# Optimization experiments

Measured on AMD Instinct MI355X. Metric: run time of the kernel, lower is better.

## Reference

```python
import jax, jax.numpy as jnp
import numpy as np

N = 50000      # nodes
E = 1600000    # edges (avg degree 32)
D_IN = 128
HID = 64


def setup_inputs() -> dict:
    key = jax.random.key(0)
    ks = jax.random.split(key, 7)
    x = jax.random.normal(ks[0], (N, D_IN), dtype=jnp.float32)
    ei = jax.random.randint(ks[1], (2, E), 0, N, dtype=jnp.int32)
    ew = jax.random.uniform(ks[2], (E,), dtype=jnp.float32)
    # GCNConv linear weights (glorot-ish scale); lin has no bias, conv bias added post-aggregation
    W1 = jax.random.normal(ks[3], (HID, D_IN), dtype=jnp.float32) * (1.0 / np.sqrt(D_IN))
    b1 = jnp.zeros((HID,), dtype=jnp.float32)
    W2 = jax.random.normal(ks[4], (HID, HID), dtype=jnp.float32) * (1.0 / np.sqrt(HID))
    b2 = jnp.zeros((HID,), dtype=jnp.float32)
    return {"x": x, "ei": ei, "ew": ew, "W1": W1, "b1": b1, "W2": W2, "b2": b2}


def _gcn_conv(x, src, dst, ew_all, W, b, n_nodes):
    """PyG GCNConv: gcn_norm (self-loops already appended) + x@W.T, gather-scale-scatter, +b."""
    deg = jax.ops.segment_sum(ew_all, dst, num_segments=n_nodes)  # dst-side weighted degree
    dinv = jnp.where(deg > 0, jax.lax.rsqrt(deg), 0.0)            # deg^{-1/2}, inf->0
    norm = dinv[src] * ew_all * dinv[dst]                          # [E+N]
    h = x @ W.T                                                    # [N, hid]
    msg = h[src] * norm[:, None]                                   # gather + scale
    out = jax.ops.segment_sum(msg, dst, num_segments=n_nodes)     # scatter-add
    return out + b


def reference(x, ei, ew, W1, b1, W2, b2):
    n_nodes = x.shape[0]
    # add self loops once (fill value 1.0), shared by both conv layers
    loop = jnp.arange(n_nodes, dtype=ei.dtype)
    src = jnp.concatenate([ei[0], loop])
    dst = jnp.concatenate([ei[1], loop])
    ew_all = jnp.concatenate([ew, jnp.ones((n_nodes,), dtype=ew.dtype)])

    h1 = jax.nn.relu(_gcn_conv(x, src, dst, ew_all, W1, b1, n_nodes))
    # dropout is identity in eval mode
    h2 = _gcn_conv(h1, src, dst, ew_all, W2, b2, n_nodes)
    return h2 + h1
```

## Files before the change

kernel.cpp:

```cpp
#include <hip/hip_runtime.h>

#define HID 64
#define DIN 128
#define NBLK 512
#define CSH 14
#define CAP (1 << CSH)

typedef unsigned long long ull;
typedef unsigned short u16;

static __device__ __forceinline__ u16 f2bf(float f) {
  unsigned u = __float_as_uint(f);
  unsigned lsb = (u >> 16) & 1u;
  u += 0x7fffu + lsb;
  return (u16)(u >> 16);
}


__global__ __launch_bounds__(512) void k_build(const int* __restrict__ src,
                                               const int* __restrict__ dst,
                                               const float* __restrict__ ew,
                                               int* __restrict__ cursor,
                                               int2* __restrict__ bufA,
                                               int E, int NBC, int chunk,
                                               const float* __restrict__ W1,
                                               const float* __restrict__ W2,
                                               float* __restrict__ WT1,
                                               float* __restrict__ WT2) {
  int b = blockIdx.x, tid = threadIdx.x;
  if (b >= NBLK) {
    int idx = (b - NBLK) * 512 + tid;
    if (idx < DIN * 64) {
      int d = idx >> 6, j = idx & 63;
      WT1[idx] = W1[j * DIN + d];
    }
    int i2 = idx - DIN * 64;
    if (i2 >= 0 && i2 < HID * 64) {
      int d = i2 >> 6, j = i2 & 63;
      WT2[i2] = W2[j * HID + d];
    }
    return;
  }
  __shared__ int h[256];
  __shared__ int cur[256];
  if (tid < 256) h[tid] = 0;
  __syncthreads();
  int e0 = b * chunk, e1 = min(E, e0 + chunk);
  for (int e = e0 + tid; e < e1; e += 512) atomicAdd(&h[dst[e] >> 8], 1);
  __syncthreads();
  if (tid < 256) {
    int c = h[tid];
    int ofs = (c > 0) ? atomicAdd(&cursor[tid], c) : 0;
    cur[tid] = (tid << CSH) + ofs;
  }
  __syncthreads();
  for (int e = e0 + tid; e < e1; e += 512) {
    int s = src[e], d = dst[e];
    float w = ew[e];
    int p = atomicAdd(&cur[d >> 8], 1);
    bufA[p] = make_int2(__float_as_int(w), (int)(((unsigned)s << 16) | (unsigned)d));
  }
}


__global__ __launch_bounds__(512) void k_passB(const int2* __restrict__ bufA,
                                               const int* __restrict__ cursor,
                                               int2* __restrict__ bufB,
                                               int* __restrict__ offs,
                                               int* __restrict__ cnt,
                                               float* __restrict__ dinv,
                                               int NBC, int N) {
  int bin = blockIdx.x, tid = threadIdx.x;
  __shared__ int h2[256];
  __shared__ int cur[256];
  __shared__ float dg[256];
  int bbase = bin << CSH;
  int m = cursor[bin];
  if (tid < 256) { h2[tid] = 0; dg[tid] = 0.f; }
  __syncthreads();
  for (int i = tid; i < m; i += 512) {
    unsigned sd = (unsigned)bufA[bbase + i].y;
    atomicAdd(&h2[sd & 255], 1);
  }
  __syncthreads();
  int own = (tid < 256) ? h2[tid] : 0;
  for (int o = 1; o < 256; o <<= 1) {
    int u = 0;
    if (tid < 256 && tid >= o) u = h2[tid - o];
    __syncthreads();
    if (tid < 256) h2[tid] += u;
    __syncthreads();
  }
  int nd = (bin << 8) + tid;
  if (tid < 256) {
    int excl = h2[tid] - own;
    cur[tid] = excl;
    if (nd < N) { offs[nd] = bbase + excl; cnt[nd] = own; }
  }
  __syncthreads();
  for (int i = tid; i < m; i += 512) {
    int2 r = bufA[bbase + i];
    unsigned sd = (unsigned)r.y;
    int dl = (int)(sd & 255u);
    int p = atomicAdd(&cur[dl], 1);
    bufB[bbase + p] = r;
    atomicAdd(&dg[dl], __int_as_float(r.x));
  }
  __syncthreads();
  if (tid < 256 && nd < N) dinv[nd] = rsqrtf(1.0f + dg[tid]);
}


__global__ __launch_bounds__(256) void k_norm(int2* __restrict__ recs,
                                              const int* __restrict__ cursor,
                                              const float* __restrict__ dinv, int nslab) {
  int e = blockIdx.x * 256 + threadIdx.x;
  if (e < nslab && (e & (CAP - 1)) < cursor[e >> CSH]) {
    int2 r = recs[e];
    unsigned sd = (unsigned)r.y;
    int s = (int)(sd >> 16), d = (int)(sd & 0xffffu);
    float nrm = dinv[s] * __int_as_float(r.x) * dinv[d];
    recs[e] = make_int2(__float_as_int(nrm), s);
  }
}


template <int K>
__global__ __launch_bounds__(256) void k_gemm(const float* __restrict__ X,
                                              const float* __restrict__ WTg,
                                              u16* __restrict__ out, int n_nodes) {
  constexpr int PAD = 68;
  __shared__ float XT[64 * PAD];
  __shared__ float WL[64 * PAD];
  const int tid = threadIdx.x;
  const int n0 = blockIdx.x * 64;
  const int tx = tid & 15;
  const int ty = tid >> 4;
  float acc[4][4] = {{0.f}};

  for (int ph = 0; ph < K / 64; ++ph) {
    const int d0 = ph * 64;
    __syncthreads();
#pragma unroll
    for (int k = 0; k < 4; ++k) {
      int f = tid + k * 256;
      int r = f >> 4, q = f & 15;
      int n = n0 + r;
      float4 xv = (n < n_nodes)
        ? *reinterpret_cast<const float4*>(&X[(size_t)n * K + d0 + 4 * q])
        : make_float4(0.f, 0.f, 0.f, 0.f);
      *reinterpret_cast<float4*>(&XT[r * PAD + 4 * q]) = xv;
      float4 wv = *reinterpret_cast<const float4*>(&WTg[(size_t)(d0 + r) * 64 + 4 * q]);
      *reinterpret_cast<float4*>(&WL[r * PAD + 4 * q]) = wv;
    }
    __syncthreads();
#pragma unroll 4
    for (int dd = 0; dd < 64; dd += 4) {
      float4 xs[4], ws[4];
#pragma unroll
      for (int mi = 0; mi < 4; ++mi)
        xs[mi] = *reinterpret_cast<const float4*>(&XT[(4 * ty + mi) * PAD + dd]);
#pragma unroll
      for (int dk = 0; dk < 4; ++dk)
        ws[dk] = *reinterpret_cast<const float4*>(&WL[(dd + dk) * PAD + 4 * tx]);
#pragma unroll
      for (int mi = 0; mi < 4; ++mi) {
        float xm[4] = {xs[mi].x, xs[mi].y, xs[mi].z, xs[mi].w};
#pragma unroll
        for (int dk = 0; dk < 4; ++dk) {
          acc[mi][0] = fmaf(xm[dk], ws[dk].x, acc[mi][0]);
          acc[mi][1] = fmaf(xm[dk], ws[dk].y, acc[mi][1]);
          acc[mi][2] = fmaf(xm[dk], ws[dk].z, acc[mi][2]);
          acc[mi][3] = fmaf(xm[dk], ws[dk].w, acc[mi][3]);
        }
      }
    }
  }

#pragma unroll
  for (int mi = 0; mi < 4; ++mi) {
    int n = n0 + 4 * ty + mi;
    if (n < n_nodes) {
      ushort4 o = make_ushort4(f2bf(acc[mi][0]), f2bf(acc[mi][1]),
                               f2bf(acc[mi][2]), f2bf(acc[mi][3]));
      *reinterpret_cast<ushort4*>(&out[(size_t)n * HID + 4 * tx]) = o;
    }
  }
}


__device__ __forceinline__ void bfma8(const uint4& v, float w, float* a) {
  a[0] = fmaf(__uint_as_float(v.x << 16), w, a[0]);
  a[1] = fmaf(__uint_as_float(v.x & 0xffff0000u), w, a[1]);
  a[2] = fmaf(__uint_as_float(v.y << 16), w, a[2]);
  a[3] = fmaf(__uint_as_float(v.y & 0xffff0000u), w, a[3]);
  a[4] = fmaf(__uint_as_float(v.z << 16), w, a[4]);
  a[5] = fmaf(__uint_as_float(v.z & 0xffff0000u), w, a[5]);
  a[6] = fmaf(__uint_as_float(v.w << 16), w, a[6]);
  a[7] = fmaf(__uint_as_float(v.w & 0xffff0000u), w, a[7]);
}

__global__ __launch_bounds__(256) void k_agg(const u16* __restrict__ h,
                                             const int2* __restrict__ recs,
                                             const int* __restrict__ offs,
                                             const int* __restrict__ cnt,
                                             const float* __restrict__ dinv,
                                             const float* __restrict__ bias,
                                             const float* __restrict__ resid,
                                             float* __restrict__ out, int n_nodes, int mode) {
  int tid = threadIdx.x;
  int lane = tid & 63;
  int g = lane >> 3;
  int p8 = (lane & 7) * 8;
  int node = (blockIdx.x * 4 + (tid >> 6)) * 8 + g;
  if (node >= n_nodes) return;
  int beg = offs[node], end = beg + cnt[node];
  float di = dinv[node];

  float a[8], b[8];
  {
    uint4 v = *reinterpret_cast<const uint4*>(&h[(size_t)node * HID + p8]);
    float w = di * di;
    a[0] = __uint_as_float(v.x << 16) * w;
    a[1] = __uint_as_float(v.x & 0xffff0000u) * w;
    a[2] = __uint_as_float(v.y << 16) * w;
    a[3] = __uint_as_float(v.y & 0xffff0000u) * w;
    a[4] = __uint_as_float(v.z << 16) * w;
    a[5] = __uint_as_float(v.z & 0xffff0000u) * w;
    a[6] = __uint_as_float(v.w << 16) * w;
    a[7] = __uint_as_float(v.w & 0xffff0000u) * w;
#pragma unroll
    for (int j = 0; j < 8; ++j) b[j] = 0.f;
  }

  int i = beg;
  while (i + 8 <= end) {
    int2 r0 = recs[i];     int2 r1 = recs[i + 1];
    int2 r2 = recs[i + 2]; int2 r3 = recs[i + 3];
    int2 r4 = recs[i + 4]; int2 r5 = recs[i + 5];
    int2 r6 = recs[i + 6]; int2 r7 = recs[i + 7];
    uint4 v0 = *reinterpret_cast<const uint4*>(&h[(size_t)r0.y * HID + p8]);
    uint4 v1 = *reinterpret_cast<const uint4*>(&h[(size_t)r1.y * HID + p8]);
    uint4 v2 = *reinterpret_cast<const uint4*>(&h[(size_t)r2.y * HID + p8]);
    uint4 v3 = *reinterpret_cast<const uint4*>(&h[(size_t)r3.y * HID + p8]);
    uint4 v4 = *reinterpret_cast<const uint4*>(&h[(size_t)r4.y * HID + p8]);
    uint4 v5 = *reinterpret_cast<const uint4*>(&h[(size_t)r5.y * HID + p8]);
    uint4 v6 = *reinterpret_cast<const uint4*>(&h[(size_t)r6.y * HID + p8]);
    uint4 v7 = *reinterpret_cast<const uint4*>(&h[(size_t)r7.y * HID + p8]);
    bfma8(v0, __int_as_float(r0.x), a);
    bfma8(v1, __int_as_float(r1.x), b);
    bfma8(v2, __int_as_float(r2.x), a);
    bfma8(v3, __int_as_float(r3.x), b);
    bfma8(v4, __int_as_float(r4.x), a);
    bfma8(v5, __int_as_float(r5.x), b);
    bfma8(v6, __int_as_float(r6.x), a);
    bfma8(v7, __int_as_float(r7.x), b);
    i += 8;
  }
  if (i + 4 <= end) {
    int2 r0 = recs[i];     int2 r1 = recs[i + 1];
    int2 r2 = recs[i + 2]; int2 r3 = recs[i + 3];
    uint4 v0 = *reinterpret_cast<const uint4*>(&h[(size_t)r0.y * HID + p8]);
    uint4 v1 = *reinterpret_cast<const uint4*>(&h[(size_t)r1.y * HID + p8]);
    uint4 v2 = *reinterpret_cast<const uint4*>(&h[(size_t)r2.y * HID + p8]);
    uint4 v3 = *reinterpret_cast<const uint4*>(&h[(size_t)r3.y * HID + p8]);
    bfma8(v0, __int_as_float(r0.x), a);
    bfma8(v1, __int_as_float(r1.x), b);
    bfma8(v2, __int_as_float(r2.x), a);
    bfma8(v3, __int_as_float(r3.x), b);
    i += 4;
  }
  if (i + 2 <= end) {
    int2 r0 = recs[i];     int2 r1 = recs[i + 1];
    uint4 v0 = *reinterpret_cast<const uint4*>(&h[(size_t)r0.y * HID + p8]);
    uint4 v1 = *reinterpret_cast<const uint4*>(&h[(size_t)r1.y * HID + p8]);
    bfma8(v0, __int_as_float(r0.x), a);
    bfma8(v1, __int_as_float(r1.x), b);
    i += 2;
  }
  if (i < end) {
    int2 r0 = recs[i];
    uint4 v0 = *reinterpret_cast<const uint4*>(&h[(size_t)r0.y * HID + p8]);
    bfma8(v0, __int_as_float(r0.x), a);
  }

  float r[8];
#pragma unroll
  for (int j = 0; j < 8; ++j) r[j] = a[j] + b[j];
  float4 bb0 = *reinterpret_cast<const float4*>(&bias[p8]);
  float4 bb1 = *reinterpret_cast<const float4*>(&bias[p8 + 4]);
  r[0] += bb0.x; r[1] += bb0.y; r[2] += bb0.z; r[3] += bb0.w;
  r[4] += bb1.x; r[5] += bb1.y; r[6] += bb1.z; r[7] += bb1.w;
  if (mode == 0) {
#pragma unroll
    for (int j = 0; j < 8; ++j) r[j] = fmaxf(r[j], 0.f);
  } else {
    float4 rs0 = *reinterpret_cast<const float4*>(&resid[(size_t)node * HID + p8]);
    float4 rs1 = *reinterpret_cast<const float4*>(&resid[(size_t)node * HID + p8 + 4]);
    r[0] += rs0.x; r[1] += rs0.y; r[2] += rs0.z; r[3] += rs0.w;
    r[4] += rs1.x; r[5] += rs1.y; r[6] += rs1.z; r[7] += rs1.w;
  }
  *reinterpret_cast<float4*>(&out[(size_t)node * HID + p8]) =
      make_float4(r[0], r[1], r[2], r[3]);
  *reinterpret_cast<float4*>(&out[(size_t)node * HID + p8 + 4]) =
      make_float4(r[4], r[5], r[6], r[7]);
}


extern "C" void kernel_launch(void* const* d_in, const int* in_sizes, int n_in,
                              void* d_out, int out_size, void* d_ws, size_t ws_size,
                              hipStream_t stream) {
  const float* x  = (const float*)d_in[0];
  const int*   ei = (const int*)d_in[1];
  const float* ew = (const float*)d_in[2];
  const float* W1 = (const float*)d_in[3];
  const float* b1 = (const float*)d_in[4];
  const float* W2 = (const float*)d_in[5];
  const float* b2 = (const float*)d_in[6];
  float* out = (float*)d_out;

  const int N = in_sizes[0] / DIN;
  const int E = in_sizes[2];
  const int* src = ei;
  const int* dst = ei + E;

  const int NBC = (N + 255) >> 8;
  const int chunk = (E + NBLK - 1) / NBLK;
  const int nslab = NBC << CSH;

  char* p = (char*)d_ws;
  auto carve = [&](size_t bytes) {
    char* r = p;
    p += (bytes + 255) & ~(size_t)255;
    return r;
  };
  int*   cursor = (int*)carve(256 * 4);
  int*   offs   = (int*)carve((size_t)N * 4);
  int*   cnt    = (int*)carve((size_t)N * 4);
  float* dinv   = (float*)carve((size_t)N * 4);
  int2*  bufA   = (int2*)carve((size_t)nslab * 8);
  int2*  bufB   = (int2*)carve((size_t)nslab * 8);
  u16*   h      = (u16*)carve((size_t)N * HID * 2);
  float* h1     = (float*)carve((size_t)N * HID * 4);
  float* WT1    = (float*)carve((size_t)DIN * HID * 4);
  float* WT2    = (float*)carve((size_t)HID * HID * 4);

  int gblk = (N + 63) / 64;
  int ablk = (N + 31) / 32;
  int tblk = ((DIN + HID) * 64 + 511) / 512;

  hipMemsetAsync(cursor, 0, 256 * 4, stream);
  k_build<<<NBLK + tblk, 512, 0, stream>>>(src, dst, ew, cursor, bufA, E, NBC, chunk,
                                           W1, W2, WT1, WT2);
  k_passB<<<NBC, 512, 0, stream>>>(bufA, cursor, bufB, offs, cnt, dinv, NBC, N);
  k_norm<<<(nslab + 255) / 256, 256, 0, stream>>>(bufB, cursor, dinv, nslab);

  k_gemm<DIN><<<gblk, 256, 0, stream>>>(x, WT1, h, N);
  k_agg<<<ablk, 256, 0, stream>>>(h, bufB, offs, cnt, dinv, b1, nullptr, h1, N, 0);
  k_gemm<HID><<<gblk, 256, 0, stream>>>(h1, WT2, h, N);
  k_agg<<<ablk, 256, 0, stream>>>(h, bufB, offs, cnt, dinv, b2, h1, out, N, 1);
}
```

Measured before the change: 225.4 us.

## Shrink CSR bins to 64 nodes, fuse norm into passB, move dinv into gemm tail

Buckets are narrowed from 256 to 64 destination nodes, giving 782 bins instead of 196, so the second pass keeps its records in registers and scans with wave shuffles. Weighted degree is now accumulated with global float atomics during the build pass. dinv is computed by extra tail blocks added to the first GEMM launch, and the per-edge normalization is folded into passB, which removes the separate k_norm launch and one read-write pass over the edge records. The cost is E global atomics on deg, and each bin has capacity 4096 (CSH 12), which could overflow for skewed degree distributions.

```diff
diff --git a/kernel.cpp b/kernel.cpp
--- a/kernel.cpp
+++ b/kernel.cpp
@@ -3,8 +3,10 @@
 #define HID 64
 #define DIN 128
 #define NBLK 512
-#define CSH 14
+#define BSH 6
+#define CSH 12
 #define CAP (1 << CSH)
+#define MAXB 1024
 
 typedef unsigned long long ull;
 typedef unsigned short u16;
@@ -21,6 +23,7 @@
                                                const int* __restrict__ dst,
                                                const float* __restrict__ ew,
                                                int* __restrict__ cursor,
+                                               float* __restrict__ deg,
                                                int2* __restrict__ bufA,
                                                int E, int NBC, int chunk,
                                                const float* __restrict__ W1,
@@ -41,86 +44,86 @@
     }
     return;
   }
-  __shared__ int h[256];
-  __shared__ int cur[256];
-  if (tid < 256) h[tid] = 0;
+  __shared__ int h[MAXB];
+  __shared__ int cur[MAXB];
+  for (int t = tid; t < NBC; t += 512) h[t] = 0;
   __syncthreads();
   int e0 = b * chunk, e1 = min(E, e0 + chunk);
-  for (int e = e0 + tid; e < e1; e += 512) atomicAdd(&h[dst[e] >> 8], 1);
-  __syncthreads();
-  if (tid < 256) {
-    int c = h[tid];
-    int ofs = (c > 0) ? atomicAdd(&cursor[tid], c) : 0;
-    cur[tid] = (tid << CSH) + ofs;
+  for (int e = e0 + tid; e < e1; e += 512) atomicAdd(&h[dst[e] >> BSH], 1);
+  __syncthreads();
+  for (int t = tid; t < NBC; t += 512) {
+    int c = h[t];
+    int ofs = (c > 0) ? atomicAdd(&cursor[t], c) : 0;
+    cur[t] = (t << CSH) + ofs;
   }
   __syncthreads();
   for (int e = e0 + tid; e < e1; e += 512) {
     int s = src[e], d = dst[e];
     float w = ew[e];
-    int p = atomicAdd(&cur[d >> 8], 1);
+    int p = atomicAdd(&cur[d >> BSH], 1);
     bufA[p] = make_int2(__float_as_int(w), (int)(((unsigned)s << 16) | (unsigned)d));
+    atomicAdd(&deg[d], w);
   }
 }
 
 
 __global__ __launch_bounds__(512) void k_passB(const int2* __restrict__ bufA,
                                                const int* __restrict__ cursor,
+                                               const float* __restrict__ dinv,
                                                int2* __restrict__ bufB,
                                                int* __restrict__ offs,
                                                int* __restrict__ cnt,
-                                               float* __restrict__ dinv,
-                                               int NBC, int N) {
+                                               int N) {
   int bin = blockIdx.x, tid = threadIdx.x;
-  __shared__ int h2[256];
-  __shared__ int cur[256];
-  __shared__ float dg[256];
+  __shared__ int h2[64];
+  __shared__ int cur[64];
+  __shared__ float dld[64];
   int bbase = bin << CSH;
   int m = cursor[bin];
-  if (tid < 256) { h2[tid] = 0; dg[tid] = 0.f; }
-  __syncthreads();
-  for (int i = tid; i < m; i += 512) {
-    unsigned sd = (unsigned)bufA[bbase + i].y;
-    atomicAdd(&h2[sd & 255], 1);
-  }
-  __syncthreads();
-  int own = (tid < 256) ? h2[tid] : 0;
-  for (int o = 1; o < 256; o <<= 1) {
-    int u = 0;
-    if (tid < 256 && tid >= o) u = h2[tid - o];
-    __syncthreads();
-    if (tid < 256) h2[tid] += u;
-    __syncthreads();
-  }
-  int nd = (bin << 8) + tid;
-  if (tid < 256) {
-    int excl = h2[tid] - own;
+  if (tid < 64) h2[tid] = 0;
+  __syncthreads();
+  int2 rloc[8];
+#pragma unroll
+  for (int k = 0; k < 8; ++k) {
+    int i = tid + k * 512;
+    if (i < m) {
+      rloc[k] = bufA[bbase + i];
+      atomicAdd(&h2[(unsigned)rloc[k].y & 63u], 1);
+    }
+  }
+  __syncthreads();
+  if (tid < 64) {
+    int own = h2[tid];
+    int v = own;
+#pragma unroll
+    for (int o = 1; o < 64; o <<= 1) {
+      int u = __shfl_up(v, o, 64);
+      if (tid >= o) v += u;
+    }
+    int excl = v - own;
     cur[tid] = excl;
-    if (nd < N) { offs[nd] = bbase + excl; cnt[nd] = own; }
-  }
-  __syncthreads();
-  for (int i = tid; i < m; i += 512) {
-    int2 r = bufA[bbase + i];
-    unsigned sd = (unsigned)r.y;
-    int dl = (int)(sd & 255u);
-    int p = atomicAdd(&cur[dl], 1);
-    bufB[bbase + p] = r;
-    atomicAdd(&dg[dl], __int_as_float(r.x));
-  }
-  __syncthreads();
-  if (tid < 256 && nd < N) dinv[nd] = rsqrtf(1.0f + dg[tid]);
-}
-
-
-__global__ __launch_bounds__(256) void k_norm(int2* __restrict__ recs,
-                                              const int* __restrict__ cursor,
-                                              const float* __restrict__ dinv, int nslab) {
-  int e = blockIdx.x * 256 + threadIdx.x;
-  if (e < nslab && (e & (CAP - 1)) < cursor[e >> CSH]) {
-    int2 r = recs[e];
-    unsigned sd = (unsigned)r.y;
-    int s = (int)(sd >> 16), d = (int)(sd & 0xffffu);
-    float nrm = dinv[s] * __int_as_float(r.x) * dinv[d];
-    recs[e] = make_int2(__float_as_int(nrm), s);
+    int nd = (bin << BSH) + tid;
+    if (nd < N) {
+      offs[nd] = bbase + excl;
+      cnt[nd] = own;
+      dld[tid] = dinv[nd];
+    } else {
+      dld[tid] = 0.f;
+    }
+  }
+  __syncthreads();
+#pragma unroll
+  for (int k = 0; k < 8; ++k) {
+    int i = tid + k * 512;
+    if (i < m) {
+      int2 r = rloc[k];
+      unsigned sd = (unsigned)r.y;
+      int dl = (int)(sd & 63u);
+      int s = (int)(sd >> 16);
+      float nrm = dinv[s] * __int_as_float(r.x) * dld[dl];
+      int p = atomicAdd(&cur[dl], 1);
+      bufB[bbase + p] = make_int2(__float_as_int(nrm), s);
+    }
   }
 }
 
@@ -128,7 +131,15 @@
 template <int K>
 __global__ __launch_bounds__(256) void k_gemm(const float* __restrict__ X,
                                               const float* __restrict__ WTg,
-                                              u16* __restrict__ out, int n_nodes) {
+                                              u16* __restrict__ out, int n_nodes,
+                                              int gblk,
+                                              const float* __restrict__ deg,
+                                              float* __restrict__ dinv) {
+  if ((int)blockIdx.x >= gblk) {
+    int i = ((int)blockIdx.x - gblk) * 256 + (int)threadIdx.x;
+    if (deg && i < n_nodes) dinv[i] = rsqrtf(1.0f + deg[i]);
+    return;
+  }
   constexpr int PAD = 68;
   __shared__ float XT[64 * PAD];
   __shared__ float WL[64 * PAD];
@@ -324,7 +335,7 @@
   const int* src = ei;
   const int* dst = ei + E;
 
-  const int NBC = (N + 255) >> 8;
+  const int NBC = (N + 63) >> BSH;
   const int chunk = (E + NBLK - 1) / NBLK;
   const int nslab = NBC << CSH;
 
@@ -334,7 +345,8 @@
     p += (bytes + 255) & ~(size_t)255;
     return r;
   };
-  int*   cursor = (int*)carve(256 * 4);
+  int*   cursor = (int*)carve((size_t)MAXB * 4 + (size_t)N * 4);
+  float* deg    = (float*)((char*)cursor + (size_t)MAXB * 4);
   int*   offs   = (int*)carve((size_t)N * 4);
   int*   cnt    = (int*)carve((size_t)N * 4);
   float* dinv   = (float*)carve((size_t)N * 4);
@@ -346,17 +358,16 @@
   float* WT2    = (float*)carve((size_t)HID * HID * 4);
 
   int gblk = (N + 63) / 64;
+  int dtail = (N + 255) / 256;
   int ablk = (N + 31) / 32;
   int tblk = ((DIN + HID) * 64 + 511) / 512;
 
-  hipMemsetAsync(cursor, 0, 256 * 4, stream);
-  k_build<<<NBLK + tblk, 512, 0, stream>>>(src, dst, ew, cursor, bufA, E, NBC, chunk,
+  hipMemsetAsync(cursor, 0, (size_t)MAXB * 4 + (size_t)N * 4, stream);
+  k_build<<<NBLK + tblk, 512, 0, stream>>>(src, dst, ew, cursor, deg, bufA, E, NBC, chunk,
                                            W1, W2, WT1, WT2);
-  k_passB<<<NBC, 512, 0, stream>>>(bufA, cursor, bufB, offs, cnt, dinv, NBC, N);
-  k_norm<<<(nslab + 255) / 256, 256, 0, stream>>>(bufB, cursor, dinv, nslab);
-
-  k_gemm<DIN><<<gblk, 256, 0, stream>>>(x, WT1, h, N);
+  k_gemm<DIN><<<gblk + dtail, 256, 0, stream>>>(x, WT1, h, N, gblk, deg, dinv);
+  k_passB<<<NBC, 512, 0, stream>>>(bufA, cursor, dinv, bufB, offs, cnt, N);
   k_agg<<<ablk, 256, 0, stream>>>(h, bufB, offs, cnt, dinv, b1, nullptr, h1, N, 0);
-  k_gemm<HID><<<gblk, 256, 0, stream>>>(h1, WT2, h, N);
+  k_gemm<HID><<<gblk, 256, 0, stream>>>(h1, WT2, h, N, gblk, nullptr, nullptr);
   k_agg<<<ablk, 256, 0, stream>>>(h, bufB, offs, cnt, dinv, b2, h1, out, N, 1);
 }
```

After: 291.8 us. +29.4%, slower.

## Replace two-pass binned CSR build with global-atomic count, scan, scatter

Applied to the files above, without the earlier changes.

Replaces the bucketed two-pass counting sort (slab bins, local re-sort, separate norm pass) with a direct CSR build: per-node global atomic counts and degree sums, a per-bin prefix scan, then one scatter pass that computes the normalized weight inline. This drops the intermediate bufA round trip and the k_norm kernel, and sizes the edge buffer by E instead of fixed-capacity slabs. In exchange it issues many global atomics on cnt, deg and cur, which may contend, and k_scan serially sums bin totals in each block. Float degree atomics make the summation order nondeterministic.

```diff
diff --git a/kernel.cpp b/kernel.cpp
--- a/kernel.cpp
+++ b/kernel.cpp
@@ -2,9 +2,8 @@
 
 #define HID 64
 #define DIN 128
-#define NBLK 512
-#define CSH 14
-#define CAP (1 << CSH)
+#define KBLK 1024
+#define SBLK 1024
 
 typedef unsigned long long ull;
 typedef unsigned short u16;
@@ -17,19 +16,19 @@
 }
 
 
-__global__ __launch_bounds__(512) void k_build(const int* __restrict__ src,
-                                               const int* __restrict__ dst,
-                                               const float* __restrict__ ew,
-                                               int* __restrict__ cursor,
-                                               int2* __restrict__ bufA,
-                                               int E, int NBC, int chunk,
-                                               const float* __restrict__ W1,
-                                               const float* __restrict__ W2,
-                                               float* __restrict__ WT1,
-                                               float* __restrict__ WT2) {
+__global__ __launch_bounds__(512) void k_cnt(const int* __restrict__ dst,
+                                             const float* __restrict__ ew,
+                                             int* __restrict__ cnt,
+                                             float* __restrict__ deg,
+                                             int* __restrict__ bsum,
+                                             int E,
+                                             const float* __restrict__ W1,
+                                             const float* __restrict__ W2,
+                                             float* __restrict__ WT1,
+                                             float* __restrict__ WT2) {
   int b = blockIdx.x, tid = threadIdx.x;
-  if (b >= NBLK) {
-    int idx = (b - NBLK) * 512 + tid;
+  if (b >= KBLK) {
+    int idx = (b - KBLK) * 512 + tid;
     if (idx < DIN * 64) {
       int d = idx >> 6, j = idx & 63;
       WT1[idx] = W1[j * DIN + d];
@@ -41,86 +40,61 @@
     }
     return;
   }
-  __shared__ int h[256];
-  __shared__ int cur[256];
-  if (tid < 256) h[tid] = 0;
+  __shared__ int hb[256];
+  if (tid < 256) hb[tid] = 0;
   __syncthreads();
-  int e0 = b * chunk, e1 = min(E, e0 + chunk);
-  for (int e = e0 + tid; e < e1; e += 512) atomicAdd(&h[dst[e] >> 8], 1);
+  for (int e = b * 512 + tid; e < E; e += KBLK * 512) {
+    int d = dst[e];
+    float w = ew[e];
+    atomicAdd(&cnt[d], 1);
+    atomicAdd(&deg[d], w);
+    atomicAdd(&hb[d >> 8], 1);
+  }
   __syncthreads();
-  if (tid < 256) {
-    int c = h[tid];
-    int ofs = (c > 0) ? atomicAdd(&cursor[tid], c) : 0;
-    cur[tid] = (tid << CSH) + ofs;
-  }
+  if (tid < 256 && hb[tid] > 0) atomicAdd(&bsum[tid], hb[tid]);
+}
+
+
+__global__ __launch_bounds__(256) void k_scan(const int* __restrict__ cnt,
+                                              const float* __restrict__ deg,
+                                              const int* __restrict__ bsum,
+                                              int* __restrict__ offs,
+                                              int* __restrict__ cur,
+                                              float* __restrict__ dinv, int N) {
+  int bin = blockIdx.x, tid = threadIdx.x;
+  __shared__ int sc[256];
+  int base = 0;
+  for (int j = 0; j < bin; ++j) base += bsum[j];
+  int nd = (bin << 8) + tid;
+  int own = (nd < N) ? cnt[nd] : 0;
+  sc[tid] = own;
   __syncthreads();
-  for (int e = e0 + tid; e < e1; e += 512) {
+  for (int o = 1; o < 256; o <<= 1) {
+    int u = (tid >= o) ? sc[tid - o] : 0;
+    __syncthreads();
+    sc[tid] += u;
+    __syncthreads();
+  }
+  if (nd < N) {
+    int excl = sc[tid] - own;
+    offs[nd] = base + excl;
+    cur[nd]  = base + excl;
+    dinv[nd] = rsqrtf(1.0f + deg[nd]);
+  }
+}
+
+
+__global__ __launch_bounds__(512) void k_scat(const int* __restrict__ src,
+                                              const int* __restrict__ dst,
+                                              const float* __restrict__ ew,
+                                              const float* __restrict__ dinv,
+                                              int* __restrict__ cur,
+                                              int2* __restrict__ bufB, int E) {
+  for (int e = blockIdx.x * 512 + threadIdx.x; e < E; e += SBLK * 512) {
     int s = src[e], d = dst[e];
-    float w = ew[e];
-    int p = atomicAdd(&cur[d >> 8], 1);
-    bufA[p] = make_int2(__float_as_int(w), (int)(((unsigned)s << 16) | (unsigned)d));
-  }
-}
-
-
-__global__ __launch_bounds__(512) void k_passB(const int2* __restrict__ bufA,
-                                               const int* __restrict__ cursor,
-                                               int2* __restrict__ bufB,
-                                               int* __restrict__ offs,
-                                               int* __restrict__ cnt,
-                                               float* __restrict__ dinv,
-                                               int NBC, int N) {
-  int bin = blockIdx.x, tid = threadIdx.x;
-  __shared__ int h2[256];
-  __shared__ int cur[256];
-  __shared__ float dg[256];
-  int bbase = bin << CSH;
-  int m = cursor[bin];
-  if (tid < 256) { h2[tid] = 0; dg[tid] = 0.f; }
-  __syncthreads();
-  for (int i = tid; i < m; i += 512) {
-    unsigned sd = (unsigned)bufA[bbase + i].y;
-    atomicAdd(&h2[sd & 255], 1);
-  }
-  __syncthreads();
-  int own = (tid < 256) ? h2[tid] : 0;
-  for (int o = 1; o < 256; o <<= 1) {
-    int u = 0;
-    if (tid < 256 && tid >= o) u = h2[tid - o];
-    __syncthreads();
-    if (tid < 256) h2[tid] += u;
-    __syncthreads();
-  }
-  int nd = (bin << 8) + tid;
-  if (tid < 256) {
-    int excl = h2[tid] - own;
-    cur[tid] = excl;
-    if (nd < N) { offs[nd] = bbase + excl; cnt[nd] = own; }
-  }
-  __syncthreads();
-  for (int i = tid; i < m; i += 512) {
-    int2 r = bufA[bbase + i];
-    unsigned sd = (unsigned)r.y;
-    int dl = (int)(sd & 255u);
-    int p = atomicAdd(&cur[dl], 1);
-    bufB[bbase + p] = r;
-    atomicAdd(&dg[dl], __int_as_float(r.x));
-  }
-  __syncthreads();
-  if (tid < 256 && nd < N) dinv[nd] = rsqrtf(1.0f + dg[tid]);
-}
-
-
-__global__ __launch_bounds__(256) void k_norm(int2* __restrict__ recs,
-                                              const int* __restrict__ cursor,
-                                              const float* __restrict__ dinv, int nslab) {
-  int e = blockIdx.x * 256 + threadIdx.x;
-  if (e < nslab && (e & (CAP - 1)) < cursor[e >> CSH]) {
-    int2 r = recs[e];
-    unsigned sd = (unsigned)r.y;
-    int s = (int)(sd >> 16), d = (int)(sd & 0xffffu);
-    float nrm = dinv[s] * __int_as_float(r.x) * dinv[d];
-    recs[e] = make_int2(__float_as_int(nrm), s);
+    float nrm = dinv[s] * ew[e] * dinv[d];
+    int p = atomicAdd(&cur[d], 1);
+    bufB[p] = make_int2(__float_as_int(nrm), s);
   }
 }
 
@@ -325,8 +299,6 @@
   const int* dst = ei + E;
 
   const int NBC = (N + 255) >> 8;
-  const int chunk = (E + NBLK - 1) / NBLK;
-  const int nslab = NBC << CSH;
 
   char* p = (char*)d_ws;
   auto carve = [&](size_t bytes) {
@@ -334,12 +306,13 @@
     p += (bytes + 255) & ~(size_t)255;
     return r;
   };
-  int*   cursor = (int*)carve(256 * 4);
+  int*   cnt    = (int*)carve((size_t)N * 4 + (size_t)N * 4 + 256 * 4);
+  float* deg    = (float*)((char*)cnt + (size_t)N * 4);
+  int*   bsum   = (int*)((char*)deg + (size_t)N * 4);
   int*   offs   = (int*)carve((size_t)N * 4);
-  int*   cnt    = (int*)carve((size_t)N * 4);
+  int*   cur    = (int*)carve((size_t)N * 4);
   float* dinv   = (float*)carve((size_t)N * 4);
-  int2*  bufA   = (int2*)carve((size_t)nslab * 8);
-  int2*  bufB   = (int2*)carve((size_t)nslab * 8);
+  int2*  bufB   = (int2*)carve((size_t)E * 8);
   u16*   h      = (u16*)carve((size_t)N * HID * 2);
   float* h1     = (float*)carve((size_t)N * HID * 4);
   float* WT1    = (float*)carve((size_t)DIN * HID * 4);
@@ -349,11 +322,10 @@
   int ablk = (N + 31) / 32;
   int tblk = ((DIN + HID) * 64 + 511) / 512;
 
-  hipMemsetAsync(cursor, 0, 256 * 4, stream);
-  k_build<<<NBLK + tblk, 512, 0, stream>>>(src, dst, ew, cursor, bufA, E, NBC, chunk,
-                                           W1, W2, WT1, WT2);
-  k_passB<<<NBC, 512, 0, stream>>>(bufA, cursor, bufB, offs, cnt, dinv, NBC, N);
-  k_norm<<<(nslab + 255) / 256, 256, 0, stream>>>(bufB, cursor, dinv, nslab);
+  hipMemsetAsync(cnt, 0, (size_t)N * 8 + 256 * 4, stream);
+  k_cnt<<<KBLK + tblk, 512, 0, stream>>>(dst, ew, cnt, deg, bsum, E, W1, W2, WT1, WT2);
+  k_scan<<<NBC, 256, 0, stream>>>(cnt, deg, bsum, offs, cur, dinv, N);
+  k_scat<<<SBLK, 512, 0, stream>>>(src, dst, ew, dinv, cur, bufB, E);
 
   k_gemm<DIN><<<gblk, 256, 0, stream>>>(x, WT1, h, N);
   k_agg<<<ablk, 256, 0, stream>>>(h, bufB, offs, cnt, dinv, b1, nullptr, h1, N, 0);
```

Result: slower. 430.9 us (+91.2%).

## Drop edge-norm kernel; apply src dinv in aggregation, dst dinv at end

Applied to the files above, without the earlier changes.

Removes the separate k_norm pass that rewrote every edge record with dinv[s]*w*dinv[d]. k_passB now writes (w, src) records directly. k_agg multiplies each edge weight by a gathered dinv[src] and applies dinv[dst] once after accumulation, with the self-loop term scaled by di inside the same factoring. k_passB also moves from 512 to 1024 threads per block. This saves a kernel launch and a full read-modify-write over the edge slab, at the cost of an extra scattered 4-byte dinv load per edge in both aggregation passes.

```diff
diff --git a/kernel.cpp b/kernel.cpp
--- a/kernel.cpp
+++ b/kernel.cpp
@@ -63,13 +63,13 @@
 }
 
 
-__global__ __launch_bounds__(512) void k_passB(const int2* __restrict__ bufA,
-                                               const int* __restrict__ cursor,
-                                               int2* __restrict__ bufB,
-                                               int* __restrict__ offs,
-                                               int* __restrict__ cnt,
-                                               float* __restrict__ dinv,
-                                               int NBC, int N) {
+__global__ __launch_bounds__(1024) void k_passB(const int2* __restrict__ bufA,
+                                                const int* __restrict__ cursor,
+                                                int2* __restrict__ bufB,
+                                                int* __restrict__ offs,
+                                                int* __restrict__ cnt,
+                                                float* __restrict__ dinv,
+                                                int NBC, int N) {
   int bin = blockIdx.x, tid = threadIdx.x;
   __shared__ int h2[256];
   __shared__ int cur[256];
@@ -78,7 +78,7 @@
   int m = cursor[bin];
   if (tid < 256) { h2[tid] = 0; dg[tid] = 0.f; }
   __syncthreads();
-  for (int i = tid; i < m; i += 512) {
+  for (int i = tid; i < m; i += 1024) {
     unsigned sd = (unsigned)bufA[bbase + i].y;
     atomicAdd(&h2[sd & 255], 1);
   }
@@ -98,30 +98,16 @@
     if (nd < N) { offs[nd] = bbase + excl; cnt[nd] = own; }
   }
   __syncthreads();
-  for (int i = tid; i < m; i += 512) {
+  for (int i = tid; i < m; i += 1024) {
     int2 r = bufA[bbase + i];
     unsigned sd = (unsigned)r.y;
     int dl = (int)(sd & 255u);
     int p = atomicAdd(&cur[dl], 1);
-    bufB[bbase + p] = r;
+    bufB[bbase + p] = make_int2(r.x, (int)(sd >> 16));
     atomicAdd(&dg[dl], __int_as_float(r.x));
   }
   __syncthreads();
   if (tid < 256 && nd < N) dinv[nd] = rsqrtf(1.0f + dg[tid]);
-}
-
-
-__global__ __launch_bounds__(256) void k_norm(int2* __restrict__ recs,
-                                              const int* __restrict__ cursor,
-                                              const float* __restrict__ dinv, int nslab) {
-  int e = blockIdx.x * 256 + threadIdx.x;
-  if (e < nslab && (e & (CAP - 1)) < cursor[e >> CSH]) {
-    int2 r = recs[e];
-    unsigned sd = (unsigned)r.y;
-    int s = (int)(sd >> 16), d = (int)(sd & 0xffffu);
-    float nrm = dinv[s] * __int_as_float(r.x) * dinv[d];
-    recs[e] = make_int2(__float_as_int(nrm), s);
-  }
 }
 
 
@@ -220,15 +206,14 @@
   float a[8], b[8];
   {
     uint4 v = *reinterpret_cast<const uint4*>(&h[(size_t)node * HID + p8]);
-    float w = di * di;
-    a[0] = __uint_as_float(v.x << 16) * w;
-    a[1] = __uint_as_float(v.x & 0xffff0000u) * w;
-    a[2] = __uint_as_float(v.y << 16) * w;
-    a[3] = __uint_as_float(v.y & 0xffff0000u) * w;
-    a[4] = __uint_as_float(v.z << 16) * w;
-    a[5] = __uint_as_float(v.z & 0xffff0000u) * w;
-    a[6] = __uint_as_float(v.w << 16) * w;
-    a[7] = __uint_as_float(v.w & 0xffff0000u) * w;
+    a[0] = __uint_as_float(v.x << 16) * di;
+    a[1] = __uint_as_float(v.x & 0xffff0000u) * di;
+    a[2] = __uint_as_float(v.y << 16) * di;
+    a[3] = __uint_as_float(v.y & 0xffff0000u) * di;
+    a[4] = __uint_as_float(v.z << 16) * di;
+    a[5] = __uint_as_float(v.z & 0xffff0000u) * di;
+    a[6] = __uint_as_float(v.w << 16) * di;
+    a[7] = __uint_as_float(v.w & 0xffff0000u) * di;
 #pragma unroll
     for (int j = 0; j < 8; ++j) b[j] = 0.f;
   }
@@ -247,14 +232,22 @@
     uint4 v5 = *reinterpret_cast<const uint4*>(&h[(size_t)r5.y * HID + p8]);
     uint4 v6 = *reinterpret_cast<const uint4*>(&h[(size_t)r6.y * HID + p8]);
     uint4 v7 = *reinterpret_cast<const uint4*>(&h[(size_t)r7.y * HID + p8]);
-    bfma8(v0, __int_as_float(r0.x), a);
-    bfma8(v1, __int_as_float(r1.x), b);
-    bfma8(v2, __int_as_float(r2.x), a);
-    bfma8(v3, __int_as_float(r3.x), b);
-    bfma8(v4, __int_as_float(r4.x), a);
-    bfma8(v5, __int_as_float(r5.x), b);
-    bfma8(v6, __int_as_float(r6.x), a);
-    bfma8(v7, __int_as_float(r7.x), b);
+    float w0 = __int_as_float(r0.x) * dinv[r0.y];
+    float w1 = __int_as_float(r1.x) * dinv[r1.y];
+    float w2 = __int_as_float(r2.x) * dinv[r2.y];
+    float w3 = __int_as_float(r3.x) * dinv[r3.y];
+    float w4 = __int_as_float(r4.x) * dinv[r4.y];
+    float w5 = __int_as_float(r5.x) * dinv[r5.y];
+    float w6 = __int_as_float(r6.x) * dinv[r6.y];
+    float w7 = __int_as_float(r7.x) * dinv[r7.y];
+    bfma8(v0, w0, a);
+    bfma8(v1, w1, b);
+    bfma8(v2, w2, a);
+    bfma8(v3, w3, b);
+    bfma8(v4, w4, a);
+    bfma8(v5, w5, b);
+    bfma8(v6, w6, a);
+    bfma8(v7, w7, b);
     i += 8;
   }
   if (i + 4 <= end) {
@@ -264,29 +257,29 @@
     uint4 v1 = *reinterpret_cast<const uint4*>(&h[(size_t)r1.y * HID + p8]);
     uint4 v2 = *reinterpret_cast<const uint4*>(&h[(size_t)r2.y * HID + p8]);
     uint4 v3 = *reinterpret_cast<const uint4*>(&h[(size_t)r3.y * HID + p8]);
-    bfma8(v0, __int_as_float(r0.x), a);
-    bfma8(v1, __int_as_float(r1.x), b);
-    bfma8(v2, __int_as_float(r2.x), a);
-    bfma8(v3, __int_as_float(r3.x), b);
+    bfma8(v0, __int_as_float(r0.x) * dinv[r0.y], a);
+    bfma8(v1, __int_as_float(r1.x) * dinv[r1.y], b);
+    bfma8(v2, __int_as_float(r2.x) * dinv[r2.y], a);
+    bfma8(v3, __int_as_float(r3.x) * dinv[r3.y], b);
     i += 4;
   }
   if (i + 2 <= end) {
     int2 r0 = recs[i];     int2 r1 = recs[i + 1];
     uint4 v0 = *reinterpret_cast<const uint4*>(&h[(size_t)r0.y * HID + p8]);
     uint4 v1 = *reinterpret_cast<const uint4*>(&h[(size_t)r1.y * HID + p8]);
-    bfma8(v0, __int_as_float(r0.x), a);
-    bfma8(v1, __int_as_float(r1.x), b);
+    bfma8(v0, __int_as_float(r0.x) * dinv[r0.y], a);
+    bfma8(v1, __int_as_float(r1.x) * dinv[r1.y], b);
     i += 2;
   }
   if (i < end) {
     int2 r0 = recs[i];
     uint4 v0 = *reinterpret_cast<const uint4*>(&h[(size_t)r0.y * HID + p8]);
-    bfma8(v0, __int_as_float(r0.x), a);
+    bfma8(v0, __int_as_float(r0.x) * dinv[r0.y], a);
   }
 
   float r[8];
 #pragma unroll
-  for (int j = 0; j < 8; ++j) r[j] = a[j] + b[j];
+  for (int j = 0; j < 8; ++j) r[j] = (a[j] + b[j]) * di;
   float4 bb0 = *reinterpret_cast<const float4*>(&bias[p8]);
   float4 bb1 = *reinterpret_cast<const float4*>(&bias[p8 + 4]);
   r[0] += bb0.x; r[1] += bb0.y; r[2] += bb0.z; r[3] += bb0.w;
@@ -352,8 +345,7 @@
   hipMemsetAsync(cursor, 0, 256 * 4, stream);
   k_build<<<NBLK + tblk, 512, 0, stream>>>(src, dst, ew, cursor, bufA, E, NBC, chunk,
                                            W1, W2, WT1, WT2);
-  k_passB<<<NBC, 512, 0, stream>>>(bufA, cursor, bufB, offs, cnt, dinv, NBC, N);
-  k_norm<<<(nslab + 255) / 256, 256, 0, stream>>>(bufB, cursor, dinv, nslab);
+  k_passB<<<NBC, 1024, 0, stream>>>(bufA, cursor, bufB, offs, cnt, dinv, NBC, N);
 
   k_gemm<DIN><<<gblk, 256, 0, stream>>>(x, WT1, h, N);
   k_agg<<<ablk, 256, 0, stream>>>(h, bufB, offs, cnt, dinv, b1, nullptr, h1, N, 0);
```

After: 223.2 us. About the same (-1.0%).
